# Performance work log

Hardware: AMD Instinct MI355X
Metric: run time of the kernel (lower is better)

Reference implementation:

```python
import jax, jax.numpy as jnp
import numpy as np

N = 40000
E = 640000
IN = 1300
H = 4
C = 64
G = 64  # number of graphs in the batch
NEG_SLOPE = 0.2


def gat_conv(x, edge_index, W, att_src, att_dst, bias):
    """PyG-style GATConv with default add_self_loops=True, concat heads.
    x: [N, F_in], W: [F_in, H*C], att_src/att_dst: [H, C], bias: [H*C].
    edge_index[0]=source j, edge_index[1]=target i (messages flow j->i).
    """
    n = x.shape[0]
    h = (x @ W).reshape(n, H, C)                      # [N, H, C]
    loop = jnp.arange(n, dtype=edge_index.dtype)
    src = jnp.concatenate([edge_index[0], loop])      # [E+N]
    dst = jnp.concatenate([edge_index[1], loop])      # [E+N]
    a_src = jnp.einsum('nhc,hc->nh', h, att_src)      # [N, H]
    a_dst = jnp.einsum('nhc,hc->nh', h, att_dst)      # [N, H]
    e = jax.nn.leaky_relu(a_src[src] + a_dst[dst], NEG_SLOPE)  # [E+N, H]
    # segment softmax over incoming edges of each target node
    e_max = jax.ops.segment_max(e, dst, num_segments=n)
    e = jnp.exp(e - e_max[dst])
    denom = jax.ops.segment_sum(e, dst, num_segments=n)
    alpha = e / (denom[dst] + 1e-16)                  # [E+N, H]
    msg = h[src] * alpha[:, :, None]                  # [E+N, H, C]
    out = jax.ops.segment_sum(msg, dst, num_segments=n)  # [N, H, C]
    return out.reshape(n, H * C) + bias


def global_mean_pool(x, batch, num_graphs):
    s = jax.ops.segment_sum(x, batch, num_segments=num_graphs)
    cnt = jax.ops.segment_sum(jnp.ones((x.shape[0],), x.dtype), batch,
                              num_segments=num_graphs)
    return s / jnp.maximum(cnt, 1.0)[:, None]


def setup_inputs() -> dict:
    key = jax.random.key(0)
    ks = jax.random.split(key, 12)
    x = jax.random.normal(ks[0], (N, IN), dtype=jnp.float32)
    edge_index = jax.random.randint(ks[1], (2, E), 0, N, dtype=jnp.int64)
    batch = jnp.sort(jax.random.randint(ks[2], (N,), 0, G, dtype=jnp.int64))
    s1 = 1.0 / np.sqrt(IN)
    s2 = 1.0 / np.sqrt(H * C)
    W1 = jax.random.normal(ks[3], (IN, H * C), dtype=jnp.float32) * s1
    att_src1 = jax.random.normal(ks[4], (H, C), dtype=jnp.float32) * s2
    att_dst1 = jax.random.normal(ks[5], (H, C), dtype=jnp.float32) * s2
    b1 = jnp.zeros((H * C,), jnp.float32)
    W2 = jax.random.normal(ks[6], (H * C, H * C), dtype=jnp.float32) * s2
    att_src2 = jax.random.normal(ks[7], (H, C), dtype=jnp.float32) * s2
    att_dst2 = jax.random.normal(ks[8], (H, C), dtype=jnp.float32) * s2
    b2 = jnp.zeros((H * C,), jnp.float32)
    lin_w = jax.random.normal(ks[9], (H * C, 1), dtype=jnp.float32) * s2
    lin_b = jnp.zeros((1,), jnp.float32)
    return {"x": x, "edge_index": edge_index, "batch": batch,
            "W1": W1, "att_src1": att_src1, "att_dst1": att_dst1, "b1": b1,
            "W2": W2, "att_src2": att_src2, "att_dst2": att_dst2, "b2": b2,
            "lin_w": lin_w, "lin_b": lin_b}


def reference(x, edge_index, batch, W1, att_src1, att_dst1, b1,
              W2, att_src2, att_dst2, b2, lin_w, lin_b):
    h = jax.nn.relu(gat_conv(x, edge_index, W1, att_src1, att_dst1, b1))
    h = jax.nn.relu(gat_conv(h, edge_index, W2, att_src2, att_dst2, b2))
    p = global_mean_pool(h, batch, G)                 # [G, H*C]
    out = p @ lin_w + lin_b                           # [G, 1]
    return out.squeeze()                              # [G]
```

## Files before the change

### kernel.cpp

```cpp
#include <hip/hip_runtime.h>
#include <hip/hip_bf16.h>

#define N_NODES 40000
#define N_EDGES 640000
#define F_IN    1300
#define NH      4
#define NC      64
#define F_OUT   256
#define NG      64
#define NEG_SLOPE 0.2f

typedef short short8v __attribute__((ext_vector_type(8)));
typedef float f32x16  __attribute__((ext_vector_type(16)));

__device__ __forceinline__ float lrelu(float x) { return x >= 0.f ? x : NEG_SLOPE * x; }

__device__ __forceinline__ short f2bf(float v) {
    unsigned u = __builtin_bit_cast(unsigned, v);
    unsigned r = (u + 0x7fffu + ((u >> 16) & 1u)) >> 16;
    return (short)r;
}
__device__ __forceinline__ float bf2f(short s) {
    unsigned u = ((unsigned)(unsigned short)s) << 16;
    return __builtin_bit_cast(float, u);
}

__device__ __forceinline__ short8v ld8(const short* p) {
    short4 a = *(const short4*)(p);
    short4 b = *(const short4*)(p + 4);
    short8v r;
    r[0] = a.x; r[1] = a.y; r[2] = a.z; r[3] = a.w;
    r[4] = b.x; r[5] = b.y; r[6] = b.z; r[7] = b.w;
    return r;
}

__global__ void wsplit_kernel(const float* __restrict__ W, short* __restrict__ hi,
                              short* __restrict__ lo, int K, int Kp)
{
    int idx = blockIdx.x * 256 + threadIdx.x;
    if (idx >= F_OUT * Kp) return;
    int n = idx / Kp, k = idx - n * Kp;
    float v = (k < K) ? W[(size_t)k * F_OUT + n] : 0.f;
    short h = f2bf(v);
    short l = f2bf(v - bf2f(h));
    hi[idx] = h;
    lo[idx] = l;
}

#define BK  32
#define LDK 40

__global__ __launch_bounds__(256, 2) void gemm_mfma_kernel(
    const float* __restrict__ A, const short* __restrict__ Bth,
    const short* __restrict__ Btl, float* __restrict__ C, int K, int Kp)
{
    __shared__ short As_hi[64][LDK], As_lo[64][LDK];
    __shared__ short Bs_hi[256][LDK], Bs_lo[256][LDK];

    const int t    = threadIdx.x;
    const int lane = t & 63;
    const int wv   = t >> 6;
    const int wc   = wv * 64;
    const int bm   = blockIdx.x * 64;

    f32x16 acc[2][2];
#pragma unroll
    for (int i = 0; i < 2; ++i)
#pragma unroll
        for (int j = 0; j < 2; ++j)
#pragma unroll
            for (int r = 0; r < 16; ++r) acc[i][j][r] = 0.f;

    const int arow = t >> 2;
    const int ac   = (t & 3) * 4;
    const int bko  = (t & 3) * 8;

    for (int k0 = 0; k0 < Kp; k0 += BK) {
        __syncthreads();
#pragma unroll
        for (int p = 0; p < 2; ++p) {
            int kk = ac + p * 16;
            int gk = k0 + kk;
            float4 v = make_float4(0.f, 0.f, 0.f, 0.f);
            if (gk < K) v = *(const float4*)&A[(size_t)(bm + arow) * K + gk];
            short4 h4, l4;
            h4.x = f2bf(v.x); l4.x = f2bf(v.x - bf2f(h4.x));
            h4.y = f2bf(v.y); l4.y = f2bf(v.y - bf2f(h4.y));
            h4.z = f2bf(v.z); l4.z = f2bf(v.z - bf2f(h4.z));
            h4.w = f2bf(v.w); l4.w = f2bf(v.w - bf2f(h4.w));
            *(short4*)&As_hi[arow][kk] = h4;
            *(short4*)&As_lo[arow][kk] = l4;
        }
#pragma unroll
        for (int p = 0; p < 4; ++p) {
            int col = p * 64 + (t >> 2);
            size_t gb = (size_t)col * Kp + k0 + bko;
            short4 h0 = *(const short4*)&Bth[gb];
            short4 h1 = *(const short4*)&Bth[gb + 4];
            short4 l0 = *(const short4*)&Btl[gb];
            short4 l1 = *(const short4*)&Btl[gb + 4];
            *(short4*)&Bs_hi[col][bko]     = h0;
            *(short4*)&Bs_hi[col][bko + 4] = h1;
            *(short4*)&Bs_lo[col][bko]     = l0;
            *(short4*)&Bs_lo[col][bko + 4] = l1;
        }
        __syncthreads();
#pragma unroll
        for (int ks = 0; ks < 2; ++ks) {
            const int ko = ks * 16 + (lane >> 5) * 8;
            const int mr = lane & 31;
            short8v ah0 = ld8(&As_hi[mr][ko]);
            short8v ah1 = ld8(&As_hi[32 + mr][ko]);
            short8v al0 = ld8(&As_lo[mr][ko]);
            short8v al1 = ld8(&As_lo[32 + mr][ko]);
            short8v bh0 = ld8(&Bs_hi[wc + mr][ko]);
            short8v bh1 = ld8(&Bs_hi[wc + 32 + mr][ko]);
            short8v bl0 = ld8(&Bs_lo[wc + mr][ko]);
            short8v bl1 = ld8(&Bs_lo[wc + 32 + mr][ko]);
            acc[0][0] = __builtin_amdgcn_mfma_f32_32x32x16_bf16(ah0, bh0, acc[0][0], 0, 0, 0);
            acc[0][0] = __builtin_amdgcn_mfma_f32_32x32x16_bf16(ah0, bl0, acc[0][0], 0, 0, 0);
            acc[0][0] = __builtin_amdgcn_mfma_f32_32x32x16_bf16(al0, bh0, acc[0][0], 0, 0, 0);
            acc[0][1] = __builtin_amdgcn_mfma_f32_32x32x16_bf16(ah0, bh1, acc[0][1], 0, 0, 0);
            acc[0][1] = __builtin_amdgcn_mfma_f32_32x32x16_bf16(ah0, bl1, acc[0][1], 0, 0, 0);
            acc[0][1] = __builtin_amdgcn_mfma_f32_32x32x16_bf16(al0, bh1, acc[0][1], 0, 0, 0);
            acc[1][0] = __builtin_amdgcn_mfma_f32_32x32x16_bf16(ah1, bh0, acc[1][0], 0, 0, 0);
            acc[1][0] = __builtin_amdgcn_mfma_f32_32x32x16_bf16(ah1, bl0, acc[1][0], 0, 0, 0);
            acc[1][0] = __builtin_amdgcn_mfma_f32_32x32x16_bf16(al1, bh0, acc[1][0], 0, 0, 0);
            acc[1][1] = __builtin_amdgcn_mfma_f32_32x32x16_bf16(ah1, bh1, acc[1][1], 0, 0, 0);
            acc[1][1] = __builtin_amdgcn_mfma_f32_32x32x16_bf16(ah1, bl1, acc[1][1], 0, 0, 0);
            acc[1][1] = __builtin_amdgcn_mfma_f32_32x32x16_bf16(al1, bh1, acc[1][1], 0, 0, 0);
        }
    }
#pragma unroll
    for (int fm = 0; fm < 2; ++fm)
#pragma unroll
        for (int fn = 0; fn < 2; ++fn)
#pragma unroll
            for (int r = 0; r < 16; ++r) {
                int row = bm + fm * 32 + (r & 3) + 8 * (r >> 2) + 4 * (lane >> 5);
                int col = wc + fn * 32 + (lane & 31);
                C[(size_t)row * F_OUT + col] = acc[fm][fn][r];
            }
}

__global__ __launch_bounds__(256) void attn_coef_kernel(const float* __restrict__ h,
                                                        const float* __restrict__ att_s,
                                                        const float* __restrict__ att_d,
                                                        float* __restrict__ a_s,
                                                        float* __restrict__ a_d)
{
    const int n = blockIdx.x;
    const int t = threadIdx.x;
    const int w = t >> 6;
    const int l = t & 63;
    float hv = h[(size_t)n * F_OUT + t];
    float vs = hv * att_s[t];
    float vd = hv * att_d[t];
#pragma unroll
    for (int o = 1; o < 64; o <<= 1) {
        vs += __shfl_xor(vs, o);
        vd += __shfl_xor(vd, o);
    }
    if (l == 0) {
        a_s[n * NH + w] = vs;
        a_d[n * NH + w] = vd;
    }
}

__global__ void hist_kernel(const int* __restrict__ ei, int* __restrict__ deg)
{
    int e = blockIdx.x * blockDim.x + threadIdx.x;
    if (e < N_EDGES) atomicAdd(&deg[ei[N_EDGES + e]], 1);
}

__global__ __launch_bounds__(1024) void scan_kernel(const int* __restrict__ deg,
                                                    int* __restrict__ rowptr)
{
    __shared__ int sums[1024];
    const int t = threadIdx.x;
    const int chunk = (N_NODES + 1023) / 1024;
    int beg = t * chunk;
    int end = beg + chunk; if (end > N_NODES) end = N_NODES;
    if (beg > N_NODES) beg = N_NODES;
    int s = 0;
    for (int i = beg; i < end; ++i) s += deg[i];
    sums[t] = s;
    __syncthreads();
    for (int o = 1; o < 1024; o <<= 1) {
        int v = (t >= o) ? sums[t - o] : 0;
        __syncthreads();
        sums[t] += v;
        __syncthreads();
    }
    int run = (t == 0) ? 0 : sums[t - 1];
    for (int i = beg; i < end; ++i) { rowptr[i] = run; run += deg[i]; }
    if (t == 1023) rowptr[N_NODES] = run;
}

__global__ void scatter_kernel(const int* __restrict__ ei, int* __restrict__ cursor,
                               int* __restrict__ ssrc)
{
    int e = blockIdx.x * blockDim.x + threadIdx.x;
    if (e < N_EDGES) {
        int d = ei[N_EDGES + e];
        int pos = atomicAdd(&cursor[d], 1);
        ssrc[pos] = ei[e];
    }
}

__global__ __launch_bounds__(256) void agg_kernel(const float* __restrict__ h,
                                                  const float* __restrict__ a_s,
                                                  const float* __restrict__ a_d,
                                                  const int* __restrict__ rowptr,
                                                  const int* __restrict__ ssrc,
                                                  const float* __restrict__ bias,
                                                  float* __restrict__ out)
{
    const int n = blockIdx.x;
    const int t = threadIdx.x;
    const int w = t >> 6;
    const int l = t & 63;
    const int beg = rowptr[n];
    const int deg = rowptr[n + 1] - beg;

    __shared__ float m_s[NH], d_s[NH];
    __shared__ int   s_idx[64];
    __shared__ float s_alpha[64][NH];

    const float adn    = a_d[n * NH + w];
    const float self_e = lrelu(a_s[n * NH + w] + adn);

    float mx = self_e;
    for (int i = l; i < deg; i += 64) {
        int s = ssrc[beg + i];
        mx = fmaxf(mx, lrelu(a_s[s * NH + w] + adn));
    }
#pragma unroll
    for (int o = 1; o < 64; o <<= 1) mx = fmaxf(mx, __shfl_xor(mx, o));

    float sm = (l == 0) ? expf(self_e - mx) : 0.f;
    for (int i = l; i < deg; i += 64) {
        int s = ssrc[beg + i];
        sm += expf(lrelu(a_s[s * NH + w] + adn) - mx);
    }
#pragma unroll
    for (int o = 1; o < 64; o <<= 1) sm += __shfl_xor(sm, o);

    if (l == 0) { m_s[w] = mx; d_s[w] = sm; }
    __syncthreads();

    const float m   = m_s[w];
    const float den = d_s[w] + 1e-16f;
    float acc = expf(self_e - m) / den * h[(size_t)n * F_OUT + t];

    for (int base = 0; base < deg; base += 64) {
        int cnt = deg - base; if (cnt > 64) cnt = 64;
        if (l < cnt) {
            int s = ssrc[beg + base + l];
            if (w == 0) s_idx[l] = s;
            s_alpha[l][w] = expf(lrelu(a_s[s * NH + w] + adn) - m) / den;
        }
        __syncthreads();
        int i = 0;
        int c4 = cnt & ~3;
        for (; i < c4; i += 4) {
            int   s0 = s_idx[i],     s1 = s_idx[i + 1];
            int   s2 = s_idx[i + 2], s3 = s_idx[i + 3];
            float a0 = s_alpha[i][w],     a1 = s_alpha[i + 1][w];
            float a2 = s_alpha[i + 2][w], a3 = s_alpha[i + 3][w];
            float h0 = h[(size_t)s0 * F_OUT + t];
            float h1 = h[(size_t)s1 * F_OUT + t];
            float h2 = h[(size_t)s2 * F_OUT + t];
            float h3 = h[(size_t)s3 * F_OUT + t];
            acc += a0 * h0 + a1 * h1 + a2 * h2 + a3 * h3;
        }
        for (; i < cnt; ++i)
            acc += s_alpha[i][w] * h[(size_t)s_idx[i] * F_OUT + t];
        __syncthreads();
    }
    out[(size_t)n * F_OUT + t] = fmaxf(acc + bias[t], 0.f);
}

__global__ void ghist_kernel(const int* __restrict__ batch, int* __restrict__ gcnt)
{
    int n = blockIdx.x * blockDim.x + threadIdx.x;
    if (n < N_NODES) atomicAdd(&gcnt[batch[n]], 1);
}

__global__ __launch_bounds__(256) void pool_kernel(const float* __restrict__ x,
                                                   const int* __restrict__ gcnt,
                                                   const float* __restrict__ lin_w,
                                                   const float* __restrict__ lin_b,
                                                   float* __restrict__ out)
{
    const int g = blockIdx.x;
    const int t = threadIdx.x;
    __shared__ int s_start;
    if (t == 0) {
        int s = 0;
        for (int i = 0; i < g; ++i) s += gcnt[i];
        s_start = s;
    }
    __syncthreads();
    const int start = s_start;
    const int cnt = gcnt[g];
    float acc = 0.f;
    for (int i = 0; i < cnt; ++i) acc += x[(size_t)(start + i) * F_OUT + t];
    float p = acc / fmaxf((float)cnt, 1.f);
    float v = p * lin_w[t];
    __shared__ float red[256];
    red[t] = v;
    __syncthreads();
    for (int o = 128; o > 0; o >>= 1) {
        if (t < o) red[t] += red[t + o];
        __syncthreads();
    }
    if (t == 0) out[g] = red[0] + lin_b[0];
}

extern "C" void kernel_launch(void* const* d_in, const int* in_sizes, int n_in,
                              void* d_out, int out_size, void* d_ws, size_t ws_size,
                              hipStream_t stream)
{
    const float* x      = (const float*)d_in[0];
    const int*   ei     = (const int*)  d_in[1];
    const int*   batch  = (const int*)  d_in[2];
    const float* W1     = (const float*)d_in[3];
    const float* att_s1 = (const float*)d_in[4];
    const float* att_d1 = (const float*)d_in[5];
    const float* b1     = (const float*)d_in[6];
    const float* W2     = (const float*)d_in[7];
    const float* att_s2 = (const float*)d_in[8];
    const float* att_d2 = (const float*)d_in[9];
    const float* b2     = (const float*)d_in[10];
    const float* lin_w  = (const float*)d_in[11];
    const float* lin_b  = (const float*)d_in[12];
    float* out = (float*)d_out;

    const int Kp1 = 1312;
    const int Kp2 = 256;

    size_t off = 0;
    auto carve = [&](size_t bytes) -> void* {
        void* p = (char*)d_ws + off;
        off += (bytes + 255) & ~(size_t)255;
        return p;
    };
    float* hA     = (float*)carve((size_t)N_NODES * F_OUT * 4);
    float* hB     = (float*)carve((size_t)N_NODES * F_OUT * 4);
    float* a_s    = (float*)carve((size_t)N_NODES * NH * 4);
    float* a_d    = (float*)carve((size_t)N_NODES * NH * 4);
    int*   deg    = (int*)  carve((size_t)(N_NODES + 1) * 4);
    int*   rowptr = (int*)  carve((size_t)(N_NODES + 1) * 4);
    int*   cursor = (int*)  carve((size_t)N_NODES * 4);
    int*   ssrc   = (int*)  carve((size_t)N_EDGES * 4);
    int*   gcnt   = (int*)  carve((size_t)NG * 4);
    short* Bt1h   = (short*)carve((size_t)F_OUT * Kp1 * 2);
    short* Bt1l   = (short*)carve((size_t)F_OUT * Kp1 * 2);
    short* Bt2h   = (short*)carve((size_t)F_OUT * Kp2 * 2);
    short* Bt2l   = (short*)carve((size_t)F_OUT * Kp2 * 2);
    (void)ws_size; (void)n_in; (void)in_sizes; (void)out_size;

    hipMemsetAsync(deg, 0, (size_t)(N_NODES + 1) * 4, stream);
    hipMemsetAsync(gcnt, 0, (size_t)NG * 4, stream);
    hist_kernel<<<(N_EDGES + 255) / 256, 256, 0, stream>>>(ei, deg);
    scan_kernel<<<1, 1024, 0, stream>>>(deg, rowptr);
    hipMemcpyAsync(cursor, rowptr, (size_t)N_NODES * 4, hipMemcpyDeviceToDevice, stream);
    scatter_kernel<<<(N_EDGES + 255) / 256, 256, 0, stream>>>(ei, cursor, ssrc);
    ghist_kernel<<<(N_NODES + 255) / 256, 256, 0, stream>>>(batch, gcnt);
    wsplit_kernel<<<(F_OUT * Kp1 + 255) / 256, 256, 0, stream>>>(W1, Bt1h, Bt1l, F_IN, Kp1);
    wsplit_kernel<<<(F_OUT * Kp2 + 255) / 256, 256, 0, stream>>>(W2, Bt2h, Bt2l, F_OUT, Kp2);

    const int gblocks = N_NODES / 64;

    gemm_mfma_kernel<<<gblocks, 256, 0, stream>>>(x, Bt1h, Bt1l, hA, F_IN, Kp1);
    attn_coef_kernel<<<N_NODES, 256, 0, stream>>>(hA, att_s1, att_d1, a_s, a_d);
    agg_kernel<<<N_NODES, 256, 0, stream>>>(hA, a_s, a_d, rowptr, ssrc, b1, hB);

    gemm_mfma_kernel<<<gblocks, 256, 0, stream>>>(hB, Bt2h, Bt2l, hA, F_OUT, Kp2);
    attn_coef_kernel<<<N_NODES, 256, 0, stream>>>(hA, att_s2, att_d2, a_s, a_d);
    agg_kernel<<<N_NODES, 256, 0, stream>>>(hA, a_s, a_d, rowptr, ssrc, b2, hB);

    pool_kernel<<<NG, 256, 0, stream>>>(hB, gcnt, lin_w, lin_b, out);
}
```

Baseline: 1.235 ms.

## Load GEMM B fragments from global, double-buffer A, make aggregation wave-per-node

The GEMM no longer stages the split-bf16 weights through shared memory. Each wave loads its B fragments straight from global memory into registers, while the A tile is double-buffered in LDS with the next slice prefetched into registers, which removes one barrier per K-step and allows three blocks per CU. The aggregation kernel now assigns one 64-lane wave per destination node with float4 feature loads. This replaces the block-per-node scheme that needed shared-memory staging and barriers. The cost is redundant global B reads, since weights are no longer shared across the block's rows, and some repeated alpha computation per lane.

```diff
diff --git a/kernel.cpp b/kernel.cpp
--- a/kernel.cpp
+++ b/kernel.cpp
@@ -48,14 +48,14 @@
 }
 
 #define BK  32
-#define LDK 40
-
-__global__ __launch_bounds__(256, 2) void gemm_mfma_kernel(
+#define LDK 36
+
+__global__ __launch_bounds__(256, 3) void gemm_mfma_kernel(
     const float* __restrict__ A, const short* __restrict__ Bth,
     const short* __restrict__ Btl, float* __restrict__ C, int K, int Kp)
 {
-    __shared__ short As_hi[64][LDK], As_lo[64][LDK];
-    __shared__ short Bs_hi[256][LDK], Bs_lo[256][LDK];
+    __shared__ short As_hi[2][64][LDK];
+    __shared__ short As_lo[2][64][LDK];
 
     const int t    = threadIdx.x;
     const int lane = t & 63;
@@ -73,50 +73,70 @@
 
     const int arow = t >> 2;
     const int ac   = (t & 3) * 4;
-    const int bko  = (t & 3) * 8;
-
-    for (int k0 = 0; k0 < Kp; k0 += BK) {
+    const int mr   = lane & 31;
+    const int khalf = (lane >> 5) * 8;
+
+    const size_t abase = (size_t)(bm + arow) * K;
+    const size_t b0 = (size_t)(wc + mr) * Kp + khalf;
+    const size_t b1 = (size_t)(wc + 32 + mr) * Kp + khalf;
+
+    const int nt = Kp / BK;
+
+    float4 av0 = make_float4(0.f, 0.f, 0.f, 0.f);
+    float4 av1 = make_float4(0.f, 0.f, 0.f, 0.f);
+    if (ac < K)      av0 = *(const float4*)&A[abase + ac];
+    if (ac + 16 < K) av1 = *(const float4*)&A[abase + ac + 16];
+
+    for (int it = 0; it < nt; ++it) {
+        const int k0  = it * BK;
+        const int buf = it & 1;
+
+        const short8v bh0_0 = *(const short8v*)&Bth[b0 + k0];
+        const short8v bh0_1 = *(const short8v*)&Bth[b0 + k0 + 16];
+        const short8v bh1_0 = *(const short8v*)&Bth[b1 + k0];
+        const short8v bh1_1 = *(const short8v*)&Bth[b1 + k0 + 16];
+        const short8v bl0_0 = *(const short8v*)&Btl[b0 + k0];
+        const short8v bl0_1 = *(const short8v*)&Btl[b0 + k0 + 16];
+        const short8v bl1_0 = *(const short8v*)&Btl[b1 + k0];
+        const short8v bl1_1 = *(const short8v*)&Btl[b1 + k0 + 16];
+
+        {
+            short4 h4, l4;
+            h4.x = f2bf(av0.x); l4.x = f2bf(av0.x - bf2f(h4.x));
+            h4.y = f2bf(av0.y); l4.y = f2bf(av0.y - bf2f(h4.y));
+            h4.z = f2bf(av0.z); l4.z = f2bf(av0.z - bf2f(h4.z));
+            h4.w = f2bf(av0.w); l4.w = f2bf(av0.w - bf2f(h4.w));
+            *(short4*)&As_hi[buf][arow][ac] = h4;
+            *(short4*)&As_lo[buf][arow][ac] = l4;
+            h4.x = f2bf(av1.x); l4.x = f2bf(av1.x - bf2f(h4.x));
+            h4.y = f2bf(av1.y); l4.y = f2bf(av1.y - bf2f(h4.y));
+            h4.z = f2bf(av1.z); l4.z = f2bf(av1.z - bf2f(h4.z));
+            h4.w = f2bf(av1.w); l4.w = f2bf(av1.w - bf2f(h4.w));
+            *(short4*)&As_hi[buf][arow][ac + 16] = h4;
+            *(short4*)&As_lo[buf][arow][ac + 16] = l4;
+        }
+
+        float4 nv0 = make_float4(0.f, 0.f, 0.f, 0.f);
+        float4 nv1 = make_float4(0.f, 0.f, 0.f, 0.f);
+        if (it + 1 < nt) {
+            int gk0 = k0 + BK + ac;
+            if (gk0 < K)      nv0 = *(const float4*)&A[abase + gk0];
+            if (gk0 + 16 < K) nv1 = *(const float4*)&A[abase + gk0 + 16];
+        }
+
         __syncthreads();
-#pragma unroll
-        for (int p = 0; p < 2; ++p) {
-            int kk = ac + p * 16;
-            int gk = k0 + kk;
-            float4 v = make_float4(0.f, 0.f, 0.f, 0.f);
-            if (gk < K) v = *(const float4*)&A[(size_t)(bm + arow) * K + gk];
-            short4 h4, l4;
-            h4.x = f2bf(v.x); l4.x = f2bf(v.x - bf2f(h4.x));
-            h4.y = f2bf(v.y); l4.y = f2bf(v.y - bf2f(h4.y));
-            h4.z = f2bf(v.z); l4.z = f2bf(v.z - bf2f(h4.z));
-            h4.w = f2bf(v.w); l4.w = f2bf(v.w - bf2f(h4.w));
-            *(short4*)&As_hi[arow][kk] = h4;
-            *(short4*)&As_lo[arow][kk] = l4;
-        }
-#pragma unroll
-        for (int p = 0; p < 4; ++p) {
-            int col = p * 64 + (t >> 2);
-            size_t gb = (size_t)col * Kp + k0 + bko;
-            short4 h0 = *(const short4*)&Bth[gb];
-            short4 h1 = *(const short4*)&Bth[gb + 4];
-            short4 l0 = *(const short4*)&Btl[gb];
-            short4 l1 = *(const short4*)&Btl[gb + 4];
-            *(short4*)&Bs_hi[col][bko]     = h0;
-            *(short4*)&Bs_hi[col][bko + 4] = h1;
-            *(short4*)&Bs_lo[col][bko]     = l0;
-            *(short4*)&Bs_lo[col][bko + 4] = l1;
-        }
-        __syncthreads();
+
 #pragma unroll
         for (int ks = 0; ks < 2; ++ks) {
-            const int ko = ks * 16 + (lane >> 5) * 8;
-            const int mr = lane & 31;
-            short8v ah0 = ld8(&As_hi[mr][ko]);
-            short8v ah1 = ld8(&As_hi[32 + mr][ko]);
-            short8v al0 = ld8(&As_lo[mr][ko]);
-            short8v al1 = ld8(&As_lo[32 + mr][ko]);
-            short8v bh0 = ld8(&Bs_hi[wc + mr][ko]);
-            short8v bh1 = ld8(&Bs_hi[wc + 32 + mr][ko]);
-            short8v bl0 = ld8(&Bs_lo[wc + mr][ko]);
-            short8v bl1 = ld8(&Bs_lo[wc + 32 + mr][ko]);
+            const int ko = ks * 16 + khalf;
+            short8v ah0 = ld8(&As_hi[buf][mr][ko]);
+            short8v ah1 = ld8(&As_hi[buf][32 + mr][ko]);
+            short8v al0 = ld8(&As_lo[buf][mr][ko]);
+            short8v al1 = ld8(&As_lo[buf][32 + mr][ko]);
+            const short8v bh0 = ks ? bh0_1 : bh0_0;
+            const short8v bh1 = ks ? bh1_1 : bh1_0;
+            const short8v bl0 = ks ? bl0_1 : bl0_0;
+            const short8v bl1 = ks ? bl1_1 : bl1_0;
             acc[0][0] = __builtin_amdgcn_mfma_f32_32x32x16_bf16(ah0, bh0, acc[0][0], 0, 0, 0);
             acc[0][0] = __builtin_amdgcn_mfma_f32_32x32x16_bf16(ah0, bl0, acc[0][0], 0, 0, 0);
             acc[0][0] = __builtin_amdgcn_mfma_f32_32x32x16_bf16(al0, bh0, acc[0][0], 0, 0, 0);
@@ -130,6 +150,8 @@
             acc[1][1] = __builtin_amdgcn_mfma_f32_32x32x16_bf16(ah1, bl1, acc[1][1], 0, 0, 0);
             acc[1][1] = __builtin_amdgcn_mfma_f32_32x32x16_bf16(al1, bh1, acc[1][1], 0, 0, 0);
         }
+        av0 = nv0;
+        av1 = nv1;
     }
 #pragma unroll
     for (int fm = 0; fm < 2; ++fm)
@@ -216,69 +238,76 @@
                                                   const float* __restrict__ bias,
                                                   float* __restrict__ out)
 {
-    const int n = blockIdx.x;
-    const int t = threadIdx.x;
-    const int w = t >> 6;
-    const int l = t & 63;
+    const int wv = threadIdx.x >> 6;
+    const int n  = blockIdx.x * 4 + wv;
+    const int l  = threadIdx.x & 63;
+    const int hd = l >> 4;
+    const int g  = l & 15;
+
     const int beg = rowptr[n];
     const int deg = rowptr[n + 1] - beg;
 
-    __shared__ float m_s[NH], d_s[NH];
-    __shared__ int   s_idx[64];
-    __shared__ float s_alpha[64][NH];
-
-    const float adn    = a_d[n * NH + w];
-    const float self_e = lrelu(a_s[n * NH + w] + adn);
+    const float adn    = a_d[n * NH + hd];
+    const float self_e = lrelu(a_s[n * NH + hd] + adn);
 
     float mx = self_e;
-    for (int i = l; i < deg; i += 64) {
+    for (int i = g; i < deg; i += 16) {
         int s = ssrc[beg + i];
-        mx = fmaxf(mx, lrelu(a_s[s * NH + w] + adn));
-    }
-#pragma unroll
-    for (int o = 1; o < 64; o <<= 1) mx = fmaxf(mx, __shfl_xor(mx, o));
-
-    float sm = (l == 0) ? expf(self_e - mx) : 0.f;
-    for (int i = l; i < deg; i += 64) {
+        mx = fmaxf(mx, lrelu(a_s[s * NH + hd] + adn));
+    }
+#pragma unroll
+    for (int o = 1; o < 16; o <<= 1) mx = fmaxf(mx, __shfl_xor(mx, o));
+
+    float sm = (g == 0) ? expf(self_e - mx) : 0.f;
+    for (int i = g; i < deg; i += 16) {
         int s = ssrc[beg + i];
-        sm += expf(lrelu(a_s[s * NH + w] + adn) - mx);
-    }
-#pragma unroll
-    for (int o = 1; o < 64; o <<= 1) sm += __shfl_xor(sm, o);
-
-    if (l == 0) { m_s[w] = mx; d_s[w] = sm; }
-    __syncthreads();
-
-    const float m   = m_s[w];
-    const float den = d_s[w] + 1e-16f;
-    float acc = expf(self_e - m) / den * h[(size_t)n * F_OUT + t];
-
-    for (int base = 0; base < deg; base += 64) {
-        int cnt = deg - base; if (cnt > 64) cnt = 64;
-        if (l < cnt) {
-            int s = ssrc[beg + base + l];
-            if (w == 0) s_idx[l] = s;
-            s_alpha[l][w] = expf(lrelu(a_s[s * NH + w] + adn) - m) / den;
-        }
-        __syncthreads();
-        int i = 0;
-        int c4 = cnt & ~3;
-        for (; i < c4; i += 4) {
-            int   s0 = s_idx[i],     s1 = s_idx[i + 1];
-            int   s2 = s_idx[i + 2], s3 = s_idx[i + 3];
-            float a0 = s_alpha[i][w],     a1 = s_alpha[i + 1][w];
-            float a2 = s_alpha[i + 2][w], a3 = s_alpha[i + 3][w];
-            float h0 = h[(size_t)s0 * F_OUT + t];
-            float h1 = h[(size_t)s1 * F_OUT + t];
-            float h2 = h[(size_t)s2 * F_OUT + t];
-            float h3 = h[(size_t)s3 * F_OUT + t];
-            acc += a0 * h0 + a1 * h1 + a2 * h2 + a3 * h3;
-        }
-        for (; i < cnt; ++i)
-            acc += s_alpha[i][w] * h[(size_t)s_idx[i] * F_OUT + t];
-        __syncthreads();
-    }
-    out[(size_t)n * F_OUT + t] = fmaxf(acc + bias[t], 0.f);
+        sm += expf(lrelu(a_s[s * NH + hd] + adn) - mx);
+    }
+#pragma unroll
+    for (int o = 1; o < 16; o <<= 1) sm += __shfl_xor(sm, o);
+    const float den = sm + 1e-16f;
+
+    const int c0 = l * 4;
+    float4 acc;
+    {
+        float a0 = expf(self_e - mx) / den;
+        float4 hv = *(const float4*)&h[(size_t)n * F_OUT + c0];
+        acc.x = a0 * hv.x; acc.y = a0 * hv.y; acc.z = a0 * hv.z; acc.w = a0 * hv.w;
+    }
+    int i = 0;
+    for (; i + 4 <= deg; i += 4) {
+        int s0 = ssrc[beg + i];
+        int s1 = ssrc[beg + i + 1];
+        int s2 = ssrc[beg + i + 2];
+        int s3 = ssrc[beg + i + 3];
+        float e0 = a_s[s0 * NH + hd], e1 = a_s[s1 * NH + hd];
+        float e2 = a_s[s2 * NH + hd], e3 = a_s[s3 * NH + hd];
+        float4 h0 = *(const float4*)&h[(size_t)s0 * F_OUT + c0];
+        float4 h1 = *(const float4*)&h[(size_t)s1 * F_OUT + c0];
+        float4 h2 = *(const float4*)&h[(size_t)s2 * F_OUT + c0];
+        float4 h3 = *(const float4*)&h[(size_t)s3 * F_OUT + c0];
+        float a0 = expf(lrelu(e0 + adn) - mx) / den;
+        float a1 = expf(lrelu(e1 + adn) - mx) / den;
+        float a2 = expf(lrelu(e2 + adn) - mx) / den;
+        float a3 = expf(lrelu(e3 + adn) - mx) / den;
+        acc.x += a0 * h0.x + a1 * h1.x + a2 * h2.x + a3 * h3.x;
+        acc.y += a0 * h0.y + a1 * h1.y + a2 * h2.y + a3 * h3.y;
+        acc.z += a0 * h0.z + a1 * h1.z + a2 * h2.z + a3 * h3.z;
+        acc.w += a0 * h0.w + a1 * h1.w + a2 * h2.w + a3 * h3.w;
+    }
+    for (; i < deg; ++i) {
+        int s = ssrc[beg + i];
+        float a0 = expf(lrelu(a_s[s * NH + hd] + adn) - mx) / den;
+        float4 hv = *(const float4*)&h[(size_t)s * F_OUT + c0];
+        acc.x += a0 * hv.x; acc.y += a0 * hv.y; acc.z += a0 * hv.z; acc.w += a0 * hv.w;
+    }
+    float4 bv = *(const float4*)&bias[c0];
+    float4 ov;
+    ov.x = fmaxf(acc.x + bv.x, 0.f);
+    ov.y = fmaxf(acc.y + bv.y, 0.f);
+    ov.z = fmaxf(acc.z + bv.z, 0.f);
+    ov.w = fmaxf(acc.w + bv.w, 0.f);
+    *(float4*)&out[(size_t)n * F_OUT + c0] = ov;
 }
 
 __global__ void ghist_kernel(const int* __restrict__ batch, int* __restrict__ gcnt)
@@ -372,14 +401,15 @@
     wsplit_kernel<<<(F_OUT * Kp2 + 255) / 256, 256, 0, stream>>>(W2, Bt2h, Bt2l, F_OUT, Kp2);
 
     const int gblocks = N_NODES / 64;
+    const int ablocks = N_NODES / 4;
 
     gemm_mfma_kernel<<<gblocks, 256, 0, stream>>>(x, Bt1h, Bt1l, hA, F_IN, Kp1);
     attn_coef_kernel<<<N_NODES, 256, 0, stream>>>(hA, att_s1, att_d1, a_s, a_d);
-    agg_kernel<<<N_NODES, 256, 0, stream>>>(hA, a_s, a_d, rowptr, ssrc, b1, hB);
+    agg_kernel<<<ablocks, 256, 0, stream>>>(hA, a_s, a_d, rowptr, ssrc, b1, hB);
 
     gemm_mfma_kernel<<<gblocks, 256, 0, stream>>>(hB, Bt2h, Bt2l, hA, F_OUT, Kp2);
     attn_coef_kernel<<<N_NODES, 256, 0, stream>>>(hA, att_s2, att_d2, a_s, a_d);
-    agg_kernel<<<N_NODES, 256, 0, stream>>>(hA, a_s, a_d, rowptr, ssrc, b2, hB);
+    agg_kernel<<<ablocks, 256, 0, stream>>>(hA, a_s, a_d, rowptr, ssrc, b2, hB);
 
     pool_kernel<<<NG, 256, 0, stream>>>(hB, gcnt, lin_w, lin_b, out);
 }
```

Result: faster. 1.183 ms (-4.2%).
